# Kernel tuning notes

Measured on AMD Instinct MI355X. Metric: run time of the kernel, lower is better.

## Reference

```python
import jax, jax.numpy as jnp
import numpy as np

# dims (Nemotron-H 8B class mamba mixer)
HID = 4096      # hidden_size
NH = 128        # mamba_num_heads
HD = 64         # mamba_head_dim
DIN = NH * HD   # intermediate_size = 8192
G = 8           # n_groups
N = 128         # ssm_state_size
K = 4           # conv_kernel
CS = 256        # chunk_size
EPS = 1e-5
GROUP_SIZE = DIN // G
CONV_DIM = DIN + 2 * G * N           # 10240
PROJ = DIN + CONV_DIM + NH           # 18560 = gate | xBC | dt


def segment_sum(x):
    """x: [..., k] -> [..., k, k]; out[i,j] = sum_{m=j+1..i} x[m], -inf above diag."""
    k = x.shape[-1]
    xe = jnp.broadcast_to(x[..., None], x.shape + (k,))
    xe = jnp.where(jnp.tril(jnp.ones((k, k), bool), -1), xe, 0.0)
    s = jnp.cumsum(xe, axis=-2)
    return jnp.where(jnp.tril(jnp.ones((k, k), bool), 0), s, -jnp.inf)


def setup_inputs() -> dict:
    key = jax.random.key(0)
    ks = jax.random.split(key, 9)
    std = 0.02
    return {
        "hidden_states": jax.random.normal(ks[0], (2, 2048, HID), jnp.float32),
        "in_proj_w": jax.random.normal(ks[1], (PROJ, HID), jnp.float32) * std,
        "conv_w": jax.random.normal(ks[2], (CONV_DIM, 1, K), jnp.float32) * 0.1,
        "conv_b": jax.random.normal(ks[3], (CONV_DIM,), jnp.float32) * 0.01,
        "dt_bias": jax.random.uniform(ks[4], (NH,), jnp.float32, -4.0, -2.0),
        "A_log": jnp.log(jax.random.uniform(ks[5], (NH,), jnp.float32, 1.0, 16.0)),
        "D": jnp.ones((NH,), jnp.float32),
        "norm_w": jnp.ones((DIN,), jnp.float32),
        "out_proj_w": jax.random.normal(ks[8], (HID, DIN), jnp.float32) * std,
    }


def reference(hidden_states, in_proj_w, conv_w, conv_b, dt_bias, A_log, D, norm_w, out_proj_w):
    b, l, _ = hidden_states.shape
    zxbcdt = hidden_states @ in_proj_w.T                       # [b,l,PROJ]
    gate = zxbcdt[..., :DIN]
    xBC = zxbcdt[..., DIN:DIN + CONV_DIM]
    dt = zxbcdt[..., DIN + CONV_DIM:]                          # [b,l,NH]

    # causal depthwise conv1d + silu
    conv = jax.lax.conv_general_dilated(
        jnp.transpose(xBC, (0, 2, 1)), conv_w, (1,), [(K - 1, 0)],
        feature_group_count=CONV_DIM, dimension_numbers=("NCH", "OIH", "NCH"))
    xBC = jax.nn.silu(jnp.transpose(conv + conv_b[None, :, None], (0, 2, 1)))

    x = xBC[..., :DIN].reshape(b, l, NH, HD)
    B = xBC[..., DIN:DIN + G * N].reshape(b, l, G, N)
    C = xBC[..., DIN + G * N:].reshape(b, l, G, N)
    B = jnp.repeat(B, NH // G, axis=2)                         # [b,l,NH,N]
    C = jnp.repeat(C, NH // G, axis=2)

    A = -jnp.exp(A_log)                                        # [NH]
    dt = jax.nn.softplus(dt + dt_bias)                         # [b,l,NH]; limit (0,inf) is a no-op

    pad = (CS - l % CS) % CS
    def padl(t):
        return jnp.pad(t, [(0, 0), (0, pad)] + [(0, 0)] * (t.ndim - 2))

    D_res = D[None, None, :, None] * padl(x)                   # [b,L,NH,HD]
    xs = x * dt[..., None]
    Adt = A[None, None, :] * dt                                # [b,l,NH]

    nc = (l + pad) // CS
    def chunk(t):
        return padl(t).reshape((b, nc, CS) + t.shape[2:])
    xs, B, C = chunk(xs), chunk(B), chunk(C)                   # [b,c,k,h,*]
    Ac = jnp.transpose(chunk(Adt), (0, 3, 1, 2))               # [b,h,c,k]
    A_cumsum = jnp.cumsum(Ac, axis=-1)

    # 1. intra-chunk (diagonal blocks)
    L = jnp.exp(segment_sum(Ac))                               # [b,h,c,k,k]
    Gm = jnp.einsum("bcihn,bcjhn->bhcij", C, B)
    Y_diag = jnp.einsum("bhcij,bcjhd->bcihd", Gm * L, xs)

    # 2. chunk states
    decay_states = jnp.exp(A_cumsum[..., -1:] - A_cumsum)      # [b,h,c,k]
    states = jnp.einsum("bckhn,bhck,bckhd->bchdn", B, decay_states, xs)

    # 3. inter-chunk recurrence
    A_tail = jnp.pad(A_cumsum[..., -1], ((0, 0), (0, 0), (1, 0)))
    decay_chunk = jnp.exp(segment_sum(A_tail))                 # [b,h,c+1,c+1]
    states = jnp.concatenate([jnp.zeros_like(states[:, :1]), states], axis=1)
    new_states = jnp.einsum("bhzc,bchdn->bzhdn", decay_chunk, states)
    states = new_states[:, :-1]                                # [b,c,h,d,n]

    # 4. state -> output
    state_decay = jnp.exp(A_cumsum)                            # [b,h,c,k]
    Y_off = jnp.einsum("bckhn,bchdn,bhck->bckhd", C, states, state_decay)

    y = (Y_diag + Y_off).reshape(b, l + pad, NH, HD) + D_res
    y = y[:, :l].reshape(b, l, DIN)

    # gated grouped RMSNorm
    y = y * jax.nn.silu(gate)
    yg = y.reshape(b, l, G, GROUP_SIZE)
    var = jnp.mean(yg * yg, axis=-1, keepdims=True)
    y = (yg * jax.lax.rsqrt(var + EPS)).reshape(b, l, DIN) * norm_w
    return y @ out_proj_w.T
```

## Files before the change

### kernel.cpp

```cpp
#include <hip/hip_runtime.h>
#include <hip/hip_bf16.h>
#include <math.h>

#define HID 4096
#define NH 128
#define HD 64
#define DIN 8192
#define G 8
#define NSTATE 128
#define CS 256
#define GROUP_SIZE 1024
#define CONV_DIM 10240
#define PROJ 18560
#define PROJ_PAD 18688
#define BATCH 2
#define SEQ 2048
#define NT (BATCH*SEQ)
#define NC 8
#define DTSK 16

typedef __attribute__((ext_vector_type(8))) short bf16x8;
typedef __attribute__((ext_vector_type(4))) float f32x4;
typedef __attribute__((ext_vector_type(8))) unsigned short u16x8;
typedef __attribute__((ext_vector_type(4))) unsigned short u16x4;

__device__ __forceinline__ float sigmoidf_(float x){ return 1.f/(1.f+expf(-x)); }
__device__ __forceinline__ float siluf_(float x){ return x*sigmoidf_(x); }
__device__ __forceinline__ float softplusf_(float x){ return (x>20.f)? x : log1pf(expf(x)); }
__device__ __forceinline__ float b2f(unsigned short u){ union{unsigned int i; float f;} x; x.i = ((unsigned int)u)<<16; return x.f; }
__device__ __forceinline__ unsigned short f2b(float f){ __hip_bfloat16 h = __float2bfloat16(f); return *(unsigned short*)&h; }

__device__ __forceinline__ void gload_lds16(const void* g, void* l) {
  __builtin_amdgcn_global_load_lds((const __attribute__((address_space(1))) unsigned int*)g,
                                   (__attribute__((address_space(3))) unsigned int*)l, 16, 0, 0);
}
__device__ __forceinline__ bf16x8 ld8bf(const __hip_bfloat16* p){ return *(const bf16x8*)p; }

__global__ __launch_bounds__(256)
void cast_f32_bf16_kernel(const float* __restrict__ in, __hip_bfloat16* __restrict__ out, size_t n8) {
  size_t i = (size_t)blockIdx.x * 256 + threadIdx.x;
  size_t stride = (size_t)gridDim.x * 256;
  for (; i < n8; i += stride) {
    const float4* p = (const float4*)(in + i*8);
    float4 a = p[0], b = p[1];
    union { __hip_bfloat16 h[8]; int4 v; } o;
    o.h[0]=__float2bfloat16(a.x); o.h[1]=__float2bfloat16(a.y);
    o.h[2]=__float2bfloat16(a.z); o.h[3]=__float2bfloat16(a.w);
    o.h[4]=__float2bfloat16(b.x); o.h[5]=__float2bfloat16(b.y);
    o.h[6]=__float2bfloat16(b.z); o.h[7]=__float2bfloat16(b.w);
    *(int4*)(out + i*8) = o.v;
  }
}

template<bool OUT_BF16, bool GUARD_N>
__global__ __launch_bounds__(512)
void gemm_bf16_256(const __hip_bfloat16* __restrict__ A, const __hip_bfloat16* __restrict__ B,
                   void* __restrict__ Cout, int M, int Nreal, int Npad, int K) {
  const int nMt = M >> 8, nNt = Npad >> 8;
  const int nwg = nMt * nNt;
  const int cpx = nwg >> 3;
  const int lin = blockIdx.x;
  const int swz = (lin & 7) * cpx + (lin >> 3);
  const int mt = swz % nMt, ntile = swz / nMt;
  const int rowBase = mt << 8;
  const int colBase = ntile << 8;

  __shared__ short As[4][8192];
  __shared__ short Bs[4][8192];

  const int tid = threadIdx.x;
  const int lane = tid & 63, wid = tid >> 6;
  const int wr = wid >> 2, wc = wid & 3;
  const int l15 = lane & 15, l4 = lane >> 4;

  const int r0 = tid >> 2,        c0 = (tid & 3) ^ ((r0 >> 1) & 3);
  const int r1 = (512+tid) >> 2,  c1 = ((512+tid) & 3) ^ ((r1 >> 1) & 3);
  const __hip_bfloat16* gA0 = A + (size_t)(rowBase + r0)*K + c0*8;
  const __hip_bfloat16* gA1 = A + (size_t)(rowBase + r1)*K + c1*8;
  const __hip_bfloat16* gB0 = B + (size_t)(colBase + r0)*K + c0*8;
  const __hip_bfloat16* gB1 = B + (size_t)(colBase + r1)*K + c1*8;
  const int ld0 = wid*512, ld1 = 4096 + wid*512;

#define STAGE_A(q, kt) do { \
    gload_lds16(gA0 + (size_t)(kt)*32, (void*)&As[q][ld0]); \
    gload_lds16(gA1 + (size_t)(kt)*32, (void*)&As[q][ld1]); \
  } while(0)
#define STAGE_B(q, kt) do { \
    gload_lds16(gB0 + (size_t)(kt)*32, (void*)&Bs[q][ld0]); \
    gload_lds16(gB1 + (size_t)(kt)*32, (void*)&Bs[q][ld1]); \
  } while(0)

  int aoff[8], boff[4];
  #pragma unroll
  for (int m=0;m<8;++m){ int r = wr*128 + m*16 + l15; aoff[m] = r*32 + ((l4 ^ ((r>>1)&3))*8); }
  #pragma unroll
  for (int n=0;n<4;++n){ int r = wc*64  + n*16 + l15; boff[n] = r*32 + ((l4 ^ ((r>>1)&3))*8); }

  f32x4 acc[8][4] = {};
  const int NKT = K >> 5;

  STAGE_A(0,0); STAGE_B(0,0);
  STAGE_A(1,1); STAGE_B(1,1);
  STAGE_A(2,2); STAGE_B(2,2);
  asm volatile("s_waitcnt vmcnt(8)" ::: "memory");
  __builtin_amdgcn_s_barrier();

  for (int t = 0; t < NKT; ++t) {
    const short* ab = &As[t&3][0];
    const short* bb = &Bs[t&3][0];
    const int q3 = (t+3)&3;
    bf16x8 a[4], b[4], a2[4];
    #pragma unroll
    for (int m=0;m<4;++m) a[m] = *(const bf16x8*)&ab[aoff[m]];
    #pragma unroll
    for (int n=0;n<4;++n) b[n] = *(const bf16x8*)&bb[boff[n]];
    if (t + 3 < NKT) STAGE_A(q3, t+3);
    __builtin_amdgcn_s_barrier();
    asm volatile("s_waitcnt lgkmcnt(0)" ::: "memory");
    __builtin_amdgcn_sched_barrier(0);
    __builtin_amdgcn_s_setprio(1);
    #pragma unroll
    for (int m=0;m<4;++m)
      #pragma unroll
      for (int n=0;n<4;++n)
        acc[m][n] = __builtin_amdgcn_mfma_f32_16x16x32_bf16(a[m], b[n], acc[m][n], 0, 0, 0);
    __builtin_amdgcn_s_setprio(0);
    __builtin_amdgcn_s_barrier();
    #pragma unroll
    for (int m=0;m<4;++m) a2[m] = *(const bf16x8*)&ab[aoff[m+4]];
    if (t + 3 < NKT) STAGE_B(q3, t+3);
    const int rem = NKT - 1 - t;
    if (rem >= 3)      asm volatile("s_waitcnt vmcnt(8)" ::: "memory");
    else if (rem == 2) asm volatile("s_waitcnt vmcnt(4)" ::: "memory");
    else if (rem == 1) asm volatile("s_waitcnt vmcnt(0)" ::: "memory");
    __builtin_amdgcn_s_barrier();
    asm volatile("s_waitcnt lgkmcnt(0)" ::: "memory");
    __builtin_amdgcn_sched_barrier(0);
    __builtin_amdgcn_s_setprio(1);
    #pragma unroll
    for (int m=0;m<4;++m)
      #pragma unroll
      for (int n=0;n<4;++n)
        acc[m+4][n] = __builtin_amdgcn_mfma_f32_16x16x32_bf16(a2[m], b[n], acc[m+4][n], 0, 0, 0);
    __builtin_amdgcn_s_setprio(0);
    __builtin_amdgcn_s_barrier();
  }
#undef STAGE_A
#undef STAGE_B

  #pragma unroll
  for (int m=0;m<8;++m) {
    int row0 = rowBase + wr*128 + m*16 + l4*4;
    #pragma unroll
    for (int n=0;n<4;++n) {
      int col = colBase + wc*64 + n*16 + l15;
      if (!GUARD_N || col < Nreal) {
        #pragma unroll
        for (int j=0;j<4;++j) {
          if (OUT_BF16)
            ((__hip_bfloat16*)Cout)[(size_t)(row0+j)*Nreal + col] = __float2bfloat16(acc[m][n][j]);
          else
            ((float*)Cout)[(size_t)(row0+j)*Nreal + col] = acc[m][n][j];
        }
      }
    }
  }
}

__global__ __launch_bounds__(256)
void dt_gemm_splitk(const float* __restrict__ A, const float* __restrict__ B,
                    float* __restrict__ partial) {
  __shared__ float As[16][132];
  __shared__ float Bs[16][132];
  const int tid = threadIdx.x;
  const int tx = tid & 15, ty = tid >> 4;
  const int rowBase = blockIdx.y * 128;
  const int k0 = blockIdx.x * (HID/DTSK);
  float acc[8][8] = {};
  for (int kt = k0; kt < k0 + HID/DTSK; kt += 16) {
    for (int e = tid; e < 128*16; e += 256) {
      int r = e >> 4, c = e & 15;
      As[c][r] = A[(size_t)(rowBase + r) * HID + kt + c];
      Bs[c][r] = B[(size_t)r * HID + kt + c];
    }
    __syncthreads();
    #pragma unroll
    for (int kk = 0; kk < 16; ++kk) {
      float a[8], bv[8];
      #pragma unroll
      for (int i = 0; i < 8; ++i) a[i] = As[kk][ty*8+i];
      #pragma unroll
      for (int j = 0; j < 8; ++j) bv[j] = Bs[kk][tx*8+j];
      #pragma unroll
      for (int i = 0; i < 8; ++i)
        #pragma unroll
        for (int j = 0; j < 8; ++j)
          acc[i][j] += a[i]*bv[j];
    }
    __syncthreads();
  }
  float* outp = partial + (size_t)blockIdx.x * NT * NH;
  for (int i = 0; i < 8; ++i) {
    size_t ro = (size_t)(rowBase + ty*8 + i) * NH + tx*8;
    #pragma unroll
    for (int j = 0; j < 8; ++j) outp[ro + j] = acc[i][j];
  }
}

__global__ __launch_bounds__(256)
void dt_reduce_kernel(const float* __restrict__ partial, float* __restrict__ dtb) {
  int idx = blockIdx.x*256 + threadIdx.x;
  float s = 0.f;
  #pragma unroll
  for (int sk = 0; sk < DTSK; ++sk) s += partial[(size_t)sk*NT*NH + idx];
  dtb[idx] = s;
}

__global__ __launch_bounds__(256)
void conv_silu_kernel(const __hip_bfloat16* __restrict__ zx, const float* __restrict__ w,
                      const float* __restrict__ bias,
                      __hip_bfloat16* __restrict__ xbf,
                      __hip_bfloat16* __restrict__ Bbf,
                      __hip_bfloat16* __restrict__ Cbf) {
  int idx = blockIdx.x * 256 + threadIdx.x;
  int c8 = idx % (CONV_DIM/8);
  int t  = idx / (CONV_DIM/8);
  int c0 = c8 * 8;
  int l = t & (SEQ-1);
  float acc[8];
  *(float4*)&acc[0] = *(const float4*)&bias[c0];
  *(float4*)&acc[4] = *(const float4*)&bias[c0+4];
  float4 wv[8];
  #pragma unroll
  for (int q=0;q<8;++q) wv[q] = *(const float4*)&w[(c0+q)*4];
  #pragma unroll
  for (int k=0;k<4;++k) {
    if (l - 3 + k >= 0) {
      u16x8 v = *(const u16x8*)&zx[(size_t)(t-3+k)*PROJ + DIN + c0];
      #pragma unroll
      for (int q=0;q<8;++q) acc[q] += b2f(v[q]) * ((const float*)&wv[q])[k];
    }
  }
  u16x8 o;
  #pragma unroll
  for (int q=0;q<8;++q) o[q] = f2b(siluf_(acc[q]));
  if (c0 < DIN) *(u16x8*)&xbf[(size_t)t*DIN + c0] = o;
  else if (c0 < DIN + G*NSTATE) *(u16x8*)&Bbf[(size_t)t*(G*NSTATE) + (c0 - DIN)] = o;
  else *(u16x8*)&Cbf[(size_t)t*(G*NSTATE) + (c0 - DIN - G*NSTATE)] = o;
}

__global__ __launch_bounds__(256)
void dt_scan_kernel(float* __restrict__ dtbuf, const float* __restrict__ dt_bias,
                    const float* __restrict__ A_log, float* __restrict__ Acs) {
  int bid = blockIdx.x;
  int c = bid % NC;
  int h = (bid / NC) % NH;
  int b = bid / (NC*NH);
  int k = threadIdx.x;
  int t = b*SEQ + c*CS + k;
  float raw = dtbuf[(size_t)t*NH + h] + dt_bias[h];
  float dtv = softplusf_(raw);
  dtbuf[(size_t)t*NH + h] = dtv;
  float adt = -expf(A_log[h]) * dtv;
  __shared__ float s[CS];
  s[k] = adt;
  __syncthreads();
  for (int off = 1; off < CS; off <<= 1) {
    float v = (k >= off) ? s[k-off] : 0.f;
    __syncthreads();
    s[k] += v;
    __syncthreads();
  }
  Acs[((size_t)(b*NH + h)*NC + c)*CS + k] = s[k];
}

__global__ __launch_bounds__(256)
void prep_xt_kernel(const __hip_bfloat16* __restrict__ xbf, const float* __restrict__ dt_sp,
                    const float* __restrict__ Acs,
                    __hip_bfloat16* __restrict__ xsT, __hip_bfloat16* __restrict__ xwT) {
  int tt = blockIdx.x;
  int h  = blockIdx.y;
  int t0 = tt*64;
  int b = t0 >> 11, cc = (t0 >> 8) & 7, k0 = t0 & 255;
  __shared__ unsigned short T[64][72];
  __shared__ float dts[64], ews[64];
  int tid = threadIdx.x;
  if (tid < 64) {
    int t = t0 + tid;
    dts[tid] = dt_sp[(size_t)t*NH + h];
    const float* acs = Acs + ((size_t)(b*NH+h)*NC + cc)*CS;
    ews[tid] = __expf(acs[CS-1] - acs[k0 + tid]);
  }
  #pragma unroll
  for (int it = 0; it < 2; ++it) {
    int r = tid >> 2;
    int c8 = (tid & 3) + it*4;
    u16x8 v = *(const u16x8*)&xbf[(size_t)(t0+r)*DIN + h*64 + c8*8];
    #pragma unroll
    for (int q=0;q<8;++q) T[c8*8+q][r] = v[q];
  }
  __syncthreads();
  #pragma unroll
  for (int it = 0; it < 2; ++it) {
    int ch = tid >> 2;
    int tc = (tid & 3) + it*4;
    u16x8 v = *(const u16x8*)&T[ch][tc*8];
    u16x8 a, wv;
    #pragma unroll
    for (int q=0;q<8;++q) {
      float f = b2f(v[q]);
      float fs = f * dts[tc*8+q];
      a[q]  = f2b(fs);
      wv[q] = f2b(fs * ews[tc*8+q]);
    }
    *(u16x8*)&xsT[(size_t)(h*64+ch)*NT + t0 + tc*8] = a;
    *(u16x8*)&xwT[(size_t)(h*64+ch)*NT + t0 + tc*8] = wv;
  }
}

__global__ __launch_bounds__(256)
void transpose_bf16_kernel(const __hip_bfloat16* __restrict__ src, __hip_bfloat16* __restrict__ dst, int S) {
  int tt = blockIdx.x;
  int ct = blockIdx.y;
  int t0 = tt*64, c0 = ct*64;
  __shared__ unsigned short T[64][72];
  int tid = threadIdx.x;
  #pragma unroll
  for (int it = 0; it < 2; ++it) {
    int r = tid >> 2;
    int c8 = (tid & 3) + it*4;
    u16x8 v = *(const u16x8*)&src[(size_t)(t0+r)*S + c0 + c8*8];
    #pragma unroll
    for (int q=0;q<8;++q) T[c8*8+q][r] = v[q];
  }
  __syncthreads();
  #pragma unroll
  for (int it = 0; it < 2; ++it) {
    int ch = tid >> 2;
    int tc = (tid & 3) + it*4;
    u16x8 v = *(const u16x8*)&T[ch][tc*8];
    *(u16x8*)&dst[(size_t)(c0+ch)*NT + t0 + tc*8] = v;
  }
}

__global__ __launch_bounds__(256)
void chunk_states_mfma(const __hip_bfloat16* __restrict__ xwT, const __hip_bfloat16* __restrict__ BT,
                       float* __restrict__ states) {
  int h = blockIdx.x, bc = blockIdx.y;
  int g = h >> 4;
  int b = bc >> 3, c = bc & 7;
  int tbase = b*SEQ + c*CS;
  int tid = threadIdx.x, lane = tid & 63, w = tid >> 6;
  int l15 = lane & 15, l4 = lane >> 4;
  int n0 = w*32;
  const __hip_bfloat16* xp = xwT + (size_t)(h*64 + l15)*NT + tbase + l4*8;
  const __hip_bfloat16* bp = BT + (size_t)(g*128 + n0 + l15)*NT + tbase + l4*8;
  f32x4 acc[4][2] = {};
  for (int kc = 0; kc < 8; ++kc) {
    bf16x8 xf[4], bf2[2];
    #pragma unroll
    for (int tm=0;tm<4;++tm) xf[tm] = ld8bf(xp + (size_t)(tm*16)*NT + kc*32);
    #pragma unroll
    for (int tn=0;tn<2;++tn) bf2[tn] = ld8bf(bp + (size_t)(tn*16)*NT + kc*32);
    #pragma unroll
    for (int tm=0;tm<4;++tm)
      #pragma unroll
      for (int tn=0;tn<2;++tn)
        acc[tm][tn] = __builtin_amdgcn_mfma_f32_16x16x32_bf16(xf[tm], bf2[tn], acc[tm][tn], 0, 0, 0);
  }
  float* out = states + ((size_t)bc*NH + h)*(HD*NSTATE);
  #pragma unroll
  for (int tm=0;tm<4;++tm)
    #pragma unroll
    for (int tn=0;tn<2;++tn)
      #pragma unroll
      for (int q=0;q<4;++q)
        out[(size_t)(tm*16 + l4*4 + q)*NSTATE + n0 + tn*16 + l15] = acc[tm][tn][q];
}

__global__ void state_recurrence_kernel(const float* __restrict__ states, const float* __restrict__ Acs,
                                        __hip_bfloat16* __restrict__ states_bf) {
  int idx = blockIdx.x*256 + threadIdx.x;
  int dn = idx & 8191;
  int h = (idx >> 13) & 127;
  int b = idx >> 20;
  float S = 0.f;
  for (int c = 0; c < NC; ++c) {
    size_t off = ((size_t)(b*NC + c)*NH + h)*8192 + dn;
    float v = states[off];
    states_bf[off] = __float2bfloat16(S);
    float decay = expf(Acs[((size_t)(b*NH+h)*NC + c)*CS + CS-1]);
    S = S*decay + v;
  }
}

__global__ __launch_bounds__(256)
void y_mfma_kernel(const __hip_bfloat16* __restrict__ zx,
                   const __hip_bfloat16* __restrict__ Cn,
                   const __hip_bfloat16* __restrict__ Bn,
                   const __hip_bfloat16* __restrict__ xsT,
                   const __hip_bfloat16* __restrict__ Sbf,
                   const float* __restrict__ dt_sp,
                   const float* __restrict__ Acs,
                   const float* __restrict__ Dp,
                   __hip_bfloat16* __restrict__ ybf) {
  int h = blockIdx.x;
  int bc = blockIdx.y;
  int c = bc & 7, b = bc >> 3;
  int g = h >> 4;
  int tbase = b*SEQ + c*CS;
  int tid = threadIdx.x, lane = tid & 63, w = tid >> 6;
  int l15 = lane & 15, l4 = lane >> 4;
  int i0 = w*64;
  __shared__ float acs_s[CS];
  __shared__ unsigned short P[4][64][72];
  acs_s[tid] = Acs[((size_t)(b*NH+h)*NC + c)*CS + tid];
  __syncthreads();

  float acs_i[4], rd[4];
  float Dh = Dp[h];
  #pragma unroll
  for (int ti=0;ti<4;++ti) {
    int ig = i0 + ti*16 + l15;
    acs_i[ti] = acs_s[ig];
    rd[ti] = Dh / dt_sp[(size_t)(tbase+ig)*NH + h];
  }
  const __hip_bfloat16* Cbase = Cn + (size_t)tbase*1024 + g*128;
  const __hip_bfloat16* Bbase = Bn + (size_t)tbase*1024 + g*128;
  const __hip_bfloat16* xbase = xsT + (size_t)(h*64 + l15)*NT + tbase;

  f32x4 accY[4][4] = {};
  for (int jb = 0; jb < 4; ++jb) {
    int j0 = jb*64;
    f32x4 sacc[4][4] = {};
    for (int kc = 0; kc < 4; ++kc) {
      bf16x8 bfr[4], cfr[4];
      #pragma unroll
      for (int tj=0;tj<4;++tj) bfr[tj] = ld8bf(Bbase + (size_t)(j0 + tj*16 + l15)*1024 + kc*32 + l4*8);
      #pragma unroll
      for (int ti=0;ti<4;++ti) cfr[ti] = ld8bf(Cbase + (size_t)(i0 + ti*16 + l15)*1024 + kc*32 + l4*8);
      #pragma unroll
      for (int tj=0;tj<4;++tj)
        #pragma unroll
        for (int ti=0;ti<4;++ti)
          sacc[tj][ti] = __builtin_amdgcn_mfma_f32_16x16x32_bf16(bfr[tj], cfr[ti], sacc[tj][ti], 0, 0, 0);
    }
    #pragma unroll
    for (int tj=0;tj<4;++tj)
      #pragma unroll
      for (int ti=0;ti<4;++ti) {
        int ig = i0 + ti*16 + l15;
        float ai = acs_i[ti];
        u16x4 pk;
        #pragma unroll
        for (int q=0;q<4;++q) {
          int jg = j0 + tj*16 + l4*4 + q;
          float v = (jg <= ig) ? sacc[tj][ti][q] * __expf(ai - acs_s[jg]) : 0.f;
          if (jg == ig) v += rd[ti];
          pk[q] = f2b(v);
        }
        *(u16x4*)&P[w][ti*16 + l15][tj*16 + l4*4] = pk;
      }
    #pragma unroll
    for (int kc2 = 0; kc2 < 2; ++kc2) {
      bf16x8 xf[4], pf[4];
      #pragma unroll
      for (int tm=0;tm<4;++tm) xf[tm] = ld8bf(xbase + (size_t)(tm*16)*NT + j0 + kc2*32 + l4*8);
      #pragma unroll
      for (int ti=0;ti<4;++ti) pf[ti] = *(const bf16x8*)&P[w][ti*16 + l15][kc2*32 + l4*8];
      #pragma unroll
      for (int tm=0;tm<4;++tm)
        #pragma unroll
        for (int ti=0;ti<4;++ti)
          accY[tm][ti] = __builtin_amdgcn_mfma_f32_16x16x32_bf16(xf[tm], pf[ti], accY[tm][ti], 0, 0, 0);
    }
  }
  const __hip_bfloat16* Sb = Sbf + ((size_t)bc*NH + h)*(HD*NSTATE);
  f32x4 oacc[4][4] = {};
  for (int kc = 0; kc < 4; ++kc) {
    bf16x8 sf[4], cfr[4];
    #pragma unroll
    for (int tm=0;tm<4;++tm) sf[tm] = ld8bf(Sb + (size_t)(tm*16 + l15)*NSTATE + kc*32 + l4*8);
    #pragma unroll
    for (int ti=0;ti<4;++ti) cfr[ti] = ld8bf(Cbase + (size_t)(i0 + ti*16 + l15)*1024 + kc*32 + l4*8);
    #pragma unroll
    for (int tm=0;tm<4;++tm)
      #pragma unroll
      for (int ti=0;ti<4;++ti)
        oacc[tm][ti] = __builtin_amdgcn_mfma_f32_16x16x32_bf16(sf[tm], cfr[ti], oacc[tm][ti], 0, 0, 0);
  }
  #pragma unroll
  for (int ti=0;ti<4;++ti) {
    int ig = i0 + ti*16 + l15;
    int t = tbase + ig;
    float sd = __expf(acs_i[ti]);
    #pragma unroll
    for (int tm=0;tm<4;++tm) {
      int ch0 = h*64 + tm*16 + l4*4;
      u16x4 gv = *(const u16x4*)&zx[(size_t)t*PROJ + ch0];
      u16x4 out;
      #pragma unroll
      for (int q=0;q<4;++q) {
        float yv = accY[tm][ti][q] + sd * oacc[tm][ti][q];
        yv *= siluf_(b2f(gv[q]));
        out[q] = f2b(yv);
      }
      *(u16x4*)&ybf[(size_t)t*DIN + ch0] = out;
    }
  }
}

__global__ __launch_bounds__(256)
void groupnorm_bf16_kernel(unsigned short* __restrict__ y, const float* __restrict__ norm_w) {
  int bid = blockIdx.x;
  int g = bid % G;
  int t = bid / G;
  unsigned short* yp = y + (size_t)t*DIN + g*GROUP_SIZE;
  int tid = threadIdx.x;
  u16x4 v = *(const u16x4*)&yp[tid*4];
  float f[4]; float ss = 0.f;
  #pragma unroll
  for (int j=0;j<4;++j) { f[j] = b2f(v[j]); ss += f[j]*f[j]; }
  #pragma unroll
  for (int off = 32; off > 0; off >>= 1) ss += __shfl_xor(ss, off);
  __shared__ float wsum[4];
  int wave = tid >> 6;
  if ((tid & 63) == 0) wsum[wave] = ss;
  __syncthreads();
  float tot = wsum[0]+wsum[1]+wsum[2]+wsum[3];
  float rs = rsqrtf(tot/(float)GROUP_SIZE + 1e-5f);
  const float* nw = norm_w + g*GROUP_SIZE + tid*4;
  u16x4 o;
  #pragma unroll
  for (int j=0;j<4;++j) o[j] = f2b(f[j] * rs * nw[j]);
  *(u16x4*)&yp[tid*4] = o;
}

extern "C" void kernel_launch(void* const* d_in, const int* in_sizes, int n_in,
                              void* d_out, int out_size, void* d_ws, size_t ws_size,
                              hipStream_t stream) {
  const float* hs        = (const float*)d_in[0];
  const float* in_proj_w = (const float*)d_in[1];
  const float* conv_w    = (const float*)d_in[2];
  const float* conv_b    = (const float*)d_in[3];
  const float* dt_bias   = (const float*)d_in[4];
  const float* A_log     = (const float*)d_in[5];
  const float* Dp        = (const float*)d_in[6];
  const float* norm_w    = (const float*)d_in[7];
  const float* out_proj_w= (const float*)d_in[8];
  float* outp = (float*)d_out;

  char* ws = (char*)d_ws;
  __hip_bfloat16* zx_bf = (__hip_bfloat16*)ws;
  char* p = ws + (size_t)NT*PROJ*2;
  __hip_bfloat16* x_bf  = (__hip_bfloat16*)p; p += (size_t)NT*DIN*2;
  __hip_bfloat16* B_bf  = (__hip_bfloat16*)p; p += (size_t)NT*G*NSTATE*2;
  __hip_bfloat16* C_bf  = (__hip_bfloat16*)p; p += (size_t)NT*G*NSTATE*2;
  __hip_bfloat16* BT    = (__hip_bfloat16*)p; p += (size_t)NT*G*NSTATE*2;
  float* states = (float*)p;  p += (size_t)BATCH*NC*NH*HD*NSTATE*4;
  __hip_bfloat16* y_bf  = (__hip_bfloat16*)p; p += (size_t)NT*DIN*2;
  float* dtb    = (float*)p;  p += (size_t)NT*NH*4;
  float* Acs    = (float*)p;  p += (size_t)BATCH*NH*NC*CS*4;
  float* dt_part = (float*)y_bf;
  char* F = p;
  __hip_bfloat16* w_in_bf   = (__hip_bfloat16*)F;
  __hip_bfloat16* xsT       = (__hip_bfloat16*)F;
  __hip_bfloat16* xwT       = (__hip_bfloat16*)(F + 67108864);
  __hip_bfloat16* hs_bf     = (__hip_bfloat16*)(F + 153092096);
  __hip_bfloat16* states_bf = (__hip_bfloat16*)(F + 153092096);
  char* F2 = F + 153092096 + 33554432;
  __hip_bfloat16* w_out_bf  = (__hip_bfloat16*)F2;

  dt_gemm_splitk<<<dim3(DTSK, NT/128), 256, 0, stream>>>(hs, in_proj_w + (size_t)(DIN+CONV_DIM)*HID, dt_part);
  dt_reduce_kernel<<<(NT*NH)/256, 256, 0, stream>>>(dt_part, dtb);

  cast_f32_bf16_kernel<<<2048, 256, 0, stream>>>(hs, hs_bf, (size_t)NT*HID/8);
  cast_f32_bf16_kernel<<<2048, 256, 0, stream>>>(in_proj_w, w_in_bf, (size_t)PROJ*HID/8);
  hipMemsetAsync(w_in_bf + (size_t)PROJ*HID, 0, (size_t)(PROJ_PAD - PROJ)*HID*2, stream);
  cast_f32_bf16_kernel<<<2048, 256, 0, stream>>>(out_proj_w, w_out_bf, (size_t)HID*DIN/8);

  gemm_bf16_256<true, true><<<dim3((NT/256)*(PROJ_PAD/256)), 512, 0, stream>>>(
      hs_bf, w_in_bf, zx_bf, NT, PROJ, PROJ_PAD, HID);

  conv_silu_kernel<<<(NT*CONV_DIM/8)/256, 256, 0, stream>>>(zx_bf, conv_w, conv_b, x_bf, B_bf, C_bf);
  dt_scan_kernel<<<BATCH*NH*NC, CS, 0, stream>>>(dtb, dt_bias, A_log, Acs);
  prep_xt_kernel<<<dim3(NT/64, NH), 256, 0, stream>>>(x_bf, dtb, Acs, xsT, xwT);
  transpose_bf16_kernel<<<dim3(NT/64, (G*NSTATE)/64), 256, 0, stream>>>(B_bf, BT, G*NSTATE);
  chunk_states_mfma<<<dim3(NH, BATCH*NC), 256, 0, stream>>>(xwT, BT, states);
  state_recurrence_kernel<<<(BATCH*NH*HD*NSTATE)/256, 256, 0, stream>>>(states, Acs, states_bf);
  y_mfma_kernel<<<dim3(NH, BATCH*NC), 256, 0, stream>>>(zx_bf, C_bf, B_bf, xsT, states_bf, dtb, Acs, Dp, y_bf);
  groupnorm_bf16_kernel<<<NT*G, 256, 0, stream>>>((unsigned short*)y_bf, norm_w);

  gemm_bf16_256<false, false><<<dim3((NT/256)*(HID/256)), 512, 0, stream>>>(
      y_bf, w_out_bf, outp, NT, HID, HID, DIN);
}
```

Measured before the change: 1.866 ms.

## Drop dt columns from bf16 in-proj GEMM, fuse casts, skip masked diag blocks

The bf16 in-projection GEMM now covers only the gate and xBC columns (18432, a multiple of 256). The dt columns are already produced by the separate fp32 split-K kernel, so the padding, the memset and the column guard are removed. The three fp32-to-bf16 casts merge into one launch. The intra-chunk y kernel limits its j-block loop to blocks at or below the diagonal (jb <= w), skipping fully masked causal blocks. This assumes w is the warp's row-block index and that masked blocks contributed zero.

```diff
diff --git a/kernel.cpp b/kernel.cpp
--- a/kernel.cpp
+++ b/kernel.cpp
@@ -11,8 +11,7 @@
 #define CS 256
 #define GROUP_SIZE 1024
 #define CONV_DIM 10240
-#define PROJ 18560
-#define PROJ_PAD 18688
+#define ZXW 18432
 #define BATCH 2
 #define SEQ 2048
 #define NT (BATCH*SEQ)
@@ -36,27 +35,39 @@
 }
 __device__ __forceinline__ bf16x8 ld8bf(const __hip_bfloat16* p){ return *(const bf16x8*)p; }
 
-__global__ __launch_bounds__(256)
-void cast_f32_bf16_kernel(const float* __restrict__ in, __hip_bfloat16* __restrict__ out, size_t n8) {
+__device__ __forceinline__ void cast8(const float* in, __hip_bfloat16* out) {
+  const float4* p = (const float4*)in;
+  float4 a = p[0], b = p[1];
+  union { __hip_bfloat16 h[8]; int4 v; } o;
+  o.h[0]=__float2bfloat16(a.x); o.h[1]=__float2bfloat16(a.y);
+  o.h[2]=__float2bfloat16(a.z); o.h[3]=__float2bfloat16(a.w);
+  o.h[4]=__float2bfloat16(b.x); o.h[5]=__float2bfloat16(b.y);
+  o.h[6]=__float2bfloat16(b.z); o.h[7]=__float2bfloat16(b.w);
+  *(int4*)out = o.v;
+}
+
+__global__ __launch_bounds__(256)
+void cast3_kernel(const float* __restrict__ hs, __hip_bfloat16* __restrict__ hs_bf,
+                  const float* __restrict__ w_in, __hip_bfloat16* __restrict__ w_in_bf,
+                  const float* __restrict__ w_out, __hip_bfloat16* __restrict__ w_out_bf) {
+  const size_t n0 = (size_t)NT*HID/8;
+  const size_t n1 = (size_t)ZXW*HID/8;
+  const size_t n2 = (size_t)HID*DIN/8;
+  const size_t ntot = n0 + n1 + n2;
   size_t i = (size_t)blockIdx.x * 256 + threadIdx.x;
   size_t stride = (size_t)gridDim.x * 256;
-  for (; i < n8; i += stride) {
-    const float4* p = (const float4*)(in + i*8);
-    float4 a = p[0], b = p[1];
-    union { __hip_bfloat16 h[8]; int4 v; } o;
-    o.h[0]=__float2bfloat16(a.x); o.h[1]=__float2bfloat16(a.y);
-    o.h[2]=__float2bfloat16(a.z); o.h[3]=__float2bfloat16(a.w);
-    o.h[4]=__float2bfloat16(b.x); o.h[5]=__float2bfloat16(b.y);
-    o.h[6]=__float2bfloat16(b.z); o.h[7]=__float2bfloat16(b.w);
-    *(int4*)(out + i*8) = o.v;
-  }
-}
-
-template<bool OUT_BF16, bool GUARD_N>
+  for (; i < ntot; i += stride) {
+    if (i < n0)            cast8(hs   + i*8,        hs_bf   + i*8);
+    else if (i < n0 + n1)  cast8(w_in + (i-n0)*8,   w_in_bf + (i-n0)*8);
+    else                   cast8(w_out+ (i-n0-n1)*8, w_out_bf+ (i-n0-n1)*8);
+  }
+}
+
+template<bool OUT_BF16>
 __global__ __launch_bounds__(512)
 void gemm_bf16_256(const __hip_bfloat16* __restrict__ A, const __hip_bfloat16* __restrict__ B,
-                   void* __restrict__ Cout, int M, int Nreal, int Npad, int K) {
-  const int nMt = M >> 8, nNt = Npad >> 8;
+                   void* __restrict__ Cout, int M, int N, int K) {
+  const int nMt = M >> 8, nNt = N >> 8;
   const int nwg = nMt * nNt;
   const int cpx = nwg >> 3;
   const int lin = blockIdx.x;
@@ -154,14 +165,12 @@
     #pragma unroll
     for (int n=0;n<4;++n) {
       int col = colBase + wc*64 + n*16 + l15;
-      if (!GUARD_N || col < Nreal) {
-        #pragma unroll
-        for (int j=0;j<4;++j) {
-          if (OUT_BF16)
-            ((__hip_bfloat16*)Cout)[(size_t)(row0+j)*Nreal + col] = __float2bfloat16(acc[m][n][j]);
-          else
-            ((float*)Cout)[(size_t)(row0+j)*Nreal + col] = acc[m][n][j];
-        }
+      #pragma unroll
+      for (int j=0;j<4;++j) {
+        if (OUT_BF16)
+          ((__hip_bfloat16*)Cout)[(size_t)(row0+j)*N + col] = __float2bfloat16(acc[m][n][j]);
+        else
+          ((float*)Cout)[(size_t)(row0+j)*N + col] = acc[m][n][j];
       }
     }
   }
@@ -236,7 +245,7 @@
   #pragma unroll
   for (int k=0;k<4;++k) {
     if (l - 3 + k >= 0) {
-      u16x8 v = *(const u16x8*)&zx[(size_t)(t-3+k)*PROJ + DIN + c0];
+      u16x8 v = *(const u16x8*)&zx[(size_t)(t-3+k)*ZXW + DIN + c0];
       #pragma unroll
       for (int q=0;q<8;++q) acc[q] += b2f(v[q]) * ((const float*)&wv[q])[k];
     }
@@ -430,7 +439,7 @@
   const __hip_bfloat16* xbase = xsT + (size_t)(h*64 + l15)*NT + tbase;
 
   f32x4 accY[4][4] = {};
-  for (int jb = 0; jb < 4; ++jb) {
+  for (int jb = 0; jb <= w; ++jb) {
     int j0 = jb*64;
     f32x4 sacc[4][4] = {};
     for (int kc = 0; kc < 4; ++kc) {
@@ -497,7 +506,7 @@
     #pragma unroll
     for (int tm=0;tm<4;++tm) {
       int ch0 = h*64 + tm*16 + l4*4;
-      u16x4 gv = *(const u16x4*)&zx[(size_t)t*PROJ + ch0];
+      u16x4 gv = *(const u16x4*)&zx[(size_t)t*ZXW + ch0];
       u16x4 out;
       #pragma unroll
       for (int q=0;q<4;++q) {
@@ -552,7 +561,7 @@
 
   char* ws = (char*)d_ws;
   __hip_bfloat16* zx_bf = (__hip_bfloat16*)ws;
-  char* p = ws + (size_t)NT*PROJ*2;
+  char* p = ws + (size_t)NT*ZXW*2;
   __hip_bfloat16* x_bf  = (__hip_bfloat16*)p; p += (size_t)NT*DIN*2;
   __hip_bfloat16* B_bf  = (__hip_bfloat16*)p; p += (size_t)NT*G*NSTATE*2;
   __hip_bfloat16* C_bf  = (__hip_bfloat16*)p; p += (size_t)NT*G*NSTATE*2;
@@ -566,21 +575,18 @@
   __hip_bfloat16* w_in_bf   = (__hip_bfloat16*)F;
   __hip_bfloat16* xsT       = (__hip_bfloat16*)F;
   __hip_bfloat16* xwT       = (__hip_bfloat16*)(F + 67108864);
-  __hip_bfloat16* hs_bf     = (__hip_bfloat16*)(F + 153092096);
-  __hip_bfloat16* states_bf = (__hip_bfloat16*)(F + 153092096);
-  char* F2 = F + 153092096 + 33554432;
+  __hip_bfloat16* hs_bf     = (__hip_bfloat16*)(F + 150994944);
+  __hip_bfloat16* states_bf = (__hip_bfloat16*)(F + 150994944);
+  char* F2 = F + 150994944 + 33554432;
   __hip_bfloat16* w_out_bf  = (__hip_bfloat16*)F2;
 
-  dt_gemm_splitk<<<dim3(DTSK, NT/128), 256, 0, stream>>>(hs, in_proj_w + (size_t)(DIN+CONV_DIM)*HID, dt_part);
+  dt_gemm_splitk<<<dim3(DTSK, NT/128), 256, 0, stream>>>(hs, in_proj_w + (size_t)ZXW*HID, dt_part);
   dt_reduce_kernel<<<(NT*NH)/256, 256, 0, stream>>>(dt_part, dtb);
 
-  cast_f32_bf16_kernel<<<2048, 256, 0, stream>>>(hs, hs_bf, (size_t)NT*HID/8);
-  cast_f32_bf16_kernel<<<2048, 256, 0, stream>>>(in_proj_w, w_in_bf, (size_t)PROJ*HID/8);
-  hipMemsetAsync(w_in_bf + (size_t)PROJ*HID, 0, (size_t)(PROJ_PAD - PROJ)*HID*2, stream);
-  cast_f32_bf16_kernel<<<2048, 256, 0, stream>>>(out_proj_w, w_out_bf, (size_t)HID*DIN/8);
-
-  gemm_bf16_256<true, true><<<dim3((NT/256)*(PROJ_PAD/256)), 512, 0, stream>>>(
-      hs_bf, w_in_bf, zx_bf, NT, PROJ, PROJ_PAD, HID);
+  cast3_kernel<<<4096, 256, 0, stream>>>(hs, hs_bf, in_proj_w, w_in_bf, out_proj_w, w_out_bf);
+
+  gemm_bf16_256<true><<<dim3((NT/256)*(ZXW/256)), 512, 0, stream>>>(
+      hs_bf, w_in_bf, zx_bf, NT, ZXW, HID);
 
   conv_silu_kernel<<<(NT*CONV_DIM/8)/256, 256, 0, stream>>>(zx_bf, conv_w, conv_b, x_bf, B_bf, C_bf);
   dt_scan_kernel<<<BATCH*NH*NC, CS, 0, stream>>>(dtb, dt_bias, A_log, Acs);
@@ -591,6 +597,6 @@
   y_mfma_kernel<<<dim3(NH, BATCH*NC), 256, 0, stream>>>(zx_bf, C_bf, B_bf, xsT, states_bf, dtb, Acs, Dp, y_bf);
   groupnorm_bf16_kernel<<<NT*G, 256, 0, stream>>>((unsigned short*)y_bf, norm_w);
 
-  gemm_bf16_256<false, false><<<dim3((NT/256)*(HID/256)), 512, 0, stream>>>(
-      y_bf, w_out_bf, outp, NT, HID, HID, DIN);
-}
+  gemm_bf16_256<false><<<dim3((NT/256)*(HID/256)), 512, 0, stream>>>(
+      y_bf, w_out_bf, outp, NT, HID, DIN);
+}
```

Result: no change. 1.889 ms (+1.3%).
